# Kernel optimization log

Hardware: AMD Instinct MI355X
Metric: run time of the kernel (lower is better)

## Reference

```python
import jax, jax.numpy as jnp
import numpy as np

EPS = 1e-5

def _bn(x, g, b, m, v):
    # inference batchnorm: (x - mean) * rsqrt(var + eps) * gamma + beta
    return (x - m) * jax.lax.rsqrt(v + EPS) * g + b

def _relu6(x):
    return jnp.clip(x, 0.0, 6.0)

def setup_inputs() -> dict:
    key = jax.random.key(0)
    ks = jax.random.split(key, 20)
    N, Cin, Cout, K = 200000, 32, 32, 9  # K = 3^2 kernel offsets (dimension=2)
    H = int(round(Cin * 6))              # hidden = in_channels * expand_ratio = 192
    inp = {}
    inp["feats"] = jax.random.normal(ks[0], (N, Cin), jnp.float32)
    # rulebook neighbor map: -1 means no active neighbor at that kernel offset
    inp["neighbor_idx"] = jax.random.randint(ks[1], (N, K), -1, N, dtype=jnp.int32)
    # ME convs have bias=False by default
    inp["W1"] = jax.random.normal(ks[2], (Cin, H), jnp.float32) * 0.05
    inp["W2"] = jax.random.normal(ks[3], (K, H), jnp.float32) * 0.05   # channelwise (depthwise) kernel
    inp["W3"] = jax.random.normal(ks[4], (H, Cout), jnp.float32) * 0.05
    for i, (name, c) in enumerate([("1", H), ("2", H), ("3", Cout)]):
        base = 5 + 4 * i
        inp["g" + name] = 1.0 + 0.1 * jax.random.normal(ks[base], (c,), jnp.float32)
        inp["b" + name] = 0.1 * jax.random.normal(ks[base + 1], (c,), jnp.float32)
        inp["m" + name] = 0.1 * jax.random.normal(ks[base + 2], (c,), jnp.float32)
        inp["v" + name] = jax.random.uniform(ks[base + 3], (c,), jnp.float32, 0.5, 1.5)
    return inp

def _depthwise_sparse_conv(x, neighbor_idx, W2):
    # x: [N, H], neighbor_idx: [N, K] (-1 = missing), W2: [K, H]
    K = W2.shape[0]
    acc = jnp.zeros_like(x)
    safe = jnp.maximum(neighbor_idx, 0)
    valid = (neighbor_idx >= 0)
    for k in range(K):  # small fixed kernel loop; each gather streams [N, H]
        g = jnp.where(valid[:, k:k + 1], x[safe[:, k]], 0.0)
        acc = acc + g * W2[k]
    return acc

def reference(feats, neighbor_idx, W1, W2, W3,
              g1, b1, m1, v1, g2, b2, m2, v2, g3, b3, m3, v3):
    identity = feats
    x = _relu6(_bn(feats @ W1, g1, b1, m1, v1))          # 1x1 expand conv
    x = _depthwise_sparse_conv(x, neighbor_idx, W2)       # 3x3 depthwise sparse conv
    x = _relu6(_bn(x, g2, b2, m2, v2))
    x = _bn(x @ W3, g3, b3, m3, v3)                       # 1x1 project conv
    return x + identity                                   # residual (in==out, stride==1)
```

## Files before the change

kernel.cpp:

```cpp
#include <hip/hip_runtime.h>

#define EPS 1e-5f

typedef __bf16 bf16x8 __attribute__((ext_vector_type(8)));
typedef float f32x4 __attribute__((ext_vector_type(4)));

union BF8 { bf16x8 v; unsigned short u[8]; uint4 q; };

__device__ inline unsigned short f32_to_bf16(float f) {
    unsigned u = __builtin_bit_cast(unsigned, f);
    return (unsigned short)((u + 0x7FFFu + ((u >> 16) & 1u)) >> 16);
}
__device__ inline float bf16_lo(unsigned u) { return __builtin_bit_cast(float, u << 16); }
__device__ inline float bf16_hi(unsigned u) { return __builtin_bit_cast(float, u & 0xFFFF0000u); }
__device__ inline float relu6f(float x) { return fminf(fmaxf(x, 0.f), 6.f); }

__global__ __launch_bounds__(256) void k1_expand(
    const float* __restrict__ feats, const float* __restrict__ W1,
    const float* __restrict__ g1, const float* __restrict__ b1,
    const float* __restrict__ m1, const float* __restrict__ v1,
    unsigned short* __restrict__ x1, int N)
{
    __shared__ __align__(16) unsigned short w1t[192 * 40];
    __shared__ __align__(16) unsigned short aT[64 * 40];
    __shared__ __align__(16) unsigned short outT[64 * 200];
    __shared__ float sL[192], bL[192];
    const int tid = threadIdx.x;
    const int rowbase = blockIdx.x * 64;

    if (tid < 192) {
        float s = g1[tid] * rsqrtf(v1[tid] + EPS);
        sL[tid] = s;
        bL[tid] = b1[tid] - m1[tid] * s;
    }

#pragma unroll
    for (int j = 0; j < 6; ++j) {
        int f = (j * 256 + tid) * 4;
        float4 w = *(const float4*)(W1 + f);
        int k = f / 192, n = f % 192;
        w1t[(n + 0) * 40 + k] = f32_to_bf16(w.x);
        w1t[(n + 1) * 40 + k] = f32_to_bf16(w.y);
        w1t[(n + 2) * 40 + k] = f32_to_bf16(w.z);
        w1t[(n + 3) * 40 + k] = f32_to_bf16(w.w);
    }

    {
        int r = tid >> 2, c = (tid & 3) * 8;
        int gr = rowbase + r;
        float4 f0 = {0.f,0.f,0.f,0.f}, f1 = {0.f,0.f,0.f,0.f};
        if (gr < N) {
            f0 = *(const float4*)(feats + (size_t)gr * 32 + c);
            f1 = *(const float4*)(feats + (size_t)gr * 32 + c + 4);
        }
        BF8 p;
        p.u[0] = f32_to_bf16(f0.x); p.u[1] = f32_to_bf16(f0.y);
        p.u[2] = f32_to_bf16(f0.z); p.u[3] = f32_to_bf16(f0.w);
        p.u[4] = f32_to_bf16(f1.x); p.u[5] = f32_to_bf16(f1.y);
        p.u[6] = f32_to_bf16(f1.z); p.u[7] = f32_to_bf16(f1.w);
        *(uint4*)(&aT[r * 40 + c]) = p.q;
    }
    __syncthreads();

    const int lane = tid & 63, wave = tid >> 6;
    const int m = lane & 15, q = lane >> 4;

    bf16x8 af = *(const bf16x8*)(&aT[(wave * 16 + m) * 40 + q * 8]);

    f32x4 acc[12];
#pragma unroll
    for (int t = 0; t < 12; ++t) {
        bf16x8 bf = *(const bf16x8*)(&w1t[(16 * t + m) * 40 + q * 8]);
        f32x4 z = {0.f, 0.f, 0.f, 0.f};
        acc[t] = __builtin_amdgcn_mfma_f32_16x16x32_bf16(af, bf, z, 0, 0, 0);
    }

#pragma unroll
    for (int t = 0; t < 12; ++t) {
        int c = 16 * t + m;
        float s = sL[c], bb = bL[c];
#pragma unroll
        for (int i = 0; i < 4; ++i) {
            int r = wave * 16 + q * 4 + i;
            outT[r * 200 + c] = f32_to_bf16(relu6f(fmaf(acc[t][i], s, bb)));
        }
    }
    __syncthreads();

#pragma unroll
    for (int j = 0; j < 6; ++j) {
        int i = j * 256 + tid;
        int r = i / 24, c = i % 24;
        int gr = rowbase + r;
        if (gr < N)
            *(uint4*)(x1 + (size_t)gr * 192 + c * 8) = *(const uint4*)(&outT[r * 200 + c * 8]);
    }
}

__global__ __launch_bounds__(192) void k2_fused(
    const unsigned short* __restrict__ x1, const int* __restrict__ nbr,
    const float* __restrict__ W2, const float* __restrict__ W3,
    const float* __restrict__ g2, const float* __restrict__ b2,
    const float* __restrict__ m2, const float* __restrict__ v2,
    const float* __restrict__ g3, const float* __restrict__ b3,
    const float* __restrict__ m3, const float* __restrict__ v3,
    const float* __restrict__ feats, float* __restrict__ out, int N)
{
    __shared__ __align__(16) unsigned short x2L[48 * 200];
    __shared__ __align__(16) int nbrL[48 * 12];
    const int tid = threadIdx.x;
    const int rowbase = blockIdx.x * 48;

    for (int i = tid; i < 432; i += 192) {
        int r = i / 9, k = i - r * 9;
        int n = rowbase + r;
        nbrL[r * 12 + k] = (n < N) ? nbr[(size_t)n * 9 + k] : -1;
    }

    const int cg = tid % 48;
    const int slot = tid / 48;
    const int c0 = cg * 4;

    float w2[9][4];
#pragma unroll
    for (int k = 0; k < 9; ++k) {
        float4 w = *(const float4*)(W2 + k * 192 + c0);
        w2[k][0] = w.x; w2[k][1] = w.y; w2[k][2] = w.z; w2[k][3] = w.w;
    }
    float s2[4], bb2[4];
#pragma unroll
    for (int j = 0; j < 4; ++j) {
        int c = c0 + j;
        s2[j] = g2[c] * rsqrtf(v2[c] + EPS);
        bb2[j] = b2[c] - m2[c] * s2[j];
    }
    __syncthreads();

#pragma unroll
    for (int it = 0; it < 12; ++it) {
        int r = it * 4 + slot;
        const int* nb = &nbrL[r * 12];
        int4 n03 = *(const int4*)nb;
        int4 n47 = *(const int4*)(nb + 4);
        int n8 = nb[8];
        int idx[9] = {n03.x, n03.y, n03.z, n03.w, n47.x, n47.y, n47.z, n47.w, n8};
        uint2 gv[9];
#pragma unroll
        for (int k = 0; k < 9; ++k) {
            int safe = idx[k] < 0 ? 0 : idx[k];
            gv[k] = *(const uint2*)(x1 + (size_t)safe * 192 + c0);
        }
        float a0 = 0.f, a1 = 0.f, a2 = 0.f, a3 = 0.f;
#pragma unroll
        for (int k = 0; k < 9; ++k) {
            unsigned ux = idx[k] >= 0 ? gv[k].x : 0u;
            unsigned uy = idx[k] >= 0 ? gv[k].y : 0u;
            a0 = fmaf(bf16_lo(ux), w2[k][0], a0);
            a1 = fmaf(bf16_hi(ux), w2[k][1], a1);
            a2 = fmaf(bf16_lo(uy), w2[k][2], a2);
            a3 = fmaf(bf16_hi(uy), w2[k][3], a3);
        }
        a0 = relu6f(fmaf(a0, s2[0], bb2[0]));
        a1 = relu6f(fmaf(a1, s2[1], bb2[1]));
        a2 = relu6f(fmaf(a2, s2[2], bb2[2]));
        a3 = relu6f(fmaf(a3, s2[3], bb2[3]));
        uint2 pk;
        pk.x = (unsigned)f32_to_bf16(a0) | ((unsigned)f32_to_bf16(a1) << 16);
        pk.y = (unsigned)f32_to_bf16(a2) | ((unsigned)f32_to_bf16(a3) << 16);
        *(uint2*)(&x2L[r * 200 + c0]) = pk;
    }
    __syncthreads();

    const int lane = tid & 63;
    const int wave = tid >> 6;
    const int m = lane & 15;
    const int q = lane >> 4;

    bf16x8 bfrag[12];
#pragma unroll
    for (int s = 0; s < 6; ++s)
#pragma unroll
        for (int t = 0; t < 2; ++t) {
            BF8 tmp;
#pragma unroll
            for (int j = 0; j < 8; ++j)
                tmp.u[j] = f32_to_bf16(W3[(32 * s + q * 8 + j) * 32 + 16 * t + m]);
            bfrag[s * 2 + t] = tmp.v;
        }

    f32x4 acc0 = {0.f, 0.f, 0.f, 0.f}, acc1 = {0.f, 0.f, 0.f, 0.f};
    const int rw = wave * 16;
#pragma unroll
    for (int s = 0; s < 6; ++s) {
        bf16x8 a = *reinterpret_cast<const bf16x8*>(&x2L[(rw + m) * 200 + 32 * s + q * 8]);
        acc0 = __builtin_amdgcn_mfma_f32_16x16x32_bf16(a, bfrag[s * 2 + 0], acc0, 0, 0, 0);
        acc1 = __builtin_amdgcn_mfma_f32_16x16x32_bf16(a, bfrag[s * 2 + 1], acc1, 0, 0, 0);
    }

#pragma unroll
    for (int t = 0; t < 2; ++t) {
        f32x4 acc = (t == 0) ? acc0 : acc1;
        int c = 16 * t + m;
        float s3  = g3[c] * rsqrtf(v3[c] + EPS);
        float bb3 = b3[c] - m3[c] * s3;
#pragma unroll
        for (int i = 0; i < 4; ++i) {
            int r = rowbase + rw + q * 4 + i;
            if (r < N) {
                int o = r * 32 + c;
                out[o] = fmaf(acc[i], s3, bb3) + feats[o];
            }
        }
    }
}

extern "C" void kernel_launch(void* const* d_in, const int* in_sizes, int n_in,
                              void* d_out, int out_size, void* d_ws, size_t ws_size,
                              hipStream_t stream) {
    const float* feats = (const float*)d_in[0];
    const int*   nbr   = (const int*)d_in[1];
    const float* W1    = (const float*)d_in[2];
    const float* W2    = (const float*)d_in[3];
    const float* W3    = (const float*)d_in[4];
    const float* g1 = (const float*)d_in[5];
    const float* b1 = (const float*)d_in[6];
    const float* m1 = (const float*)d_in[7];
    const float* v1 = (const float*)d_in[8];
    const float* g2 = (const float*)d_in[9];
    const float* b2 = (const float*)d_in[10];
    const float* m2 = (const float*)d_in[11];
    const float* v2 = (const float*)d_in[12];
    const float* g3 = (const float*)d_in[13];
    const float* b3 = (const float*)d_in[14];
    const float* m3 = (const float*)d_in[15];
    const float* v3 = (const float*)d_in[16];
    float* out = (float*)d_out;

    const int N = in_sizes[0] / 32;
    unsigned short* x1 = (unsigned short*)d_ws;

    k1_expand<<<dim3((N + 63) / 64), dim3(256), 0, stream>>>(
        feats, W1, g1, b1, m1, v1, x1, N);
    k2_fused<<<dim3((N + 47) / 48), dim3(192), 0, stream>>>(
        x1, nbr, W2, W3, g2, b2, m2, v2, g3, b3, m3, v3, feats, out, N);
}
```

Baseline: 237.1 us.

## Precompute bf16 weights and folded BN constants in a prep kernel; pair gather rows

Adds a small prep kernel that converts W1 and W3 to transposed bf16 and folds all three batchnorms into scale/bias arrays in workspace. This removes the per-block weight conversion and BN rsqrt work from the expand and fused kernels. The gather loop in k2 now handles two rows per iteration with precomputed byte offsets, giving more independent loads in flight. The cost is an extra kernel launch, global rather than LDS reads for weights, and higher register pressure in k2.

```diff
diff --git a/kernel.cpp b/kernel.cpp
--- a/kernel.cpp
+++ b/kernel.cpp
@@ -15,35 +15,50 @@
 __device__ inline float bf16_hi(unsigned u) { return __builtin_bit_cast(float, u & 0xFFFF0000u); }
 __device__ inline float relu6f(float x) { return fminf(fmaxf(x, 0.f), 6.f); }
 
-__global__ __launch_bounds__(256) void k1_expand(
-    const float* __restrict__ feats, const float* __restrict__ W1,
+__global__ __launch_bounds__(256) void k0_prep(
+    const float* __restrict__ W1, const float* __restrict__ W3,
     const float* __restrict__ g1, const float* __restrict__ b1,
     const float* __restrict__ m1, const float* __restrict__ v1,
-    unsigned short* __restrict__ x1, int N)
+    const float* __restrict__ g2, const float* __restrict__ b2,
+    const float* __restrict__ m2, const float* __restrict__ v2,
+    const float* __restrict__ g3, const float* __restrict__ b3,
+    const float* __restrict__ m3, const float* __restrict__ v3,
+    unsigned short* __restrict__ w1t, unsigned short* __restrict__ w3t,
+    float* __restrict__ bnc)
 {
-    __shared__ __align__(16) unsigned short w1t[192 * 40];
+    const int gtid = blockIdx.x * 256 + threadIdx.x;
+    const int gstr = gridDim.x * 256;
+    for (int i = gtid; i < 6144; i += gstr) {
+        int n = i >> 5, k = i & 31;
+        w1t[i] = f32_to_bf16(W1[k * 192 + n]);
+    }
+    for (int i = gtid; i < 6144; i += gstr) {
+        int n = i / 192, k = i - n * 192;
+        w3t[i] = f32_to_bf16(W3[k * 32 + n]);
+    }
+    if (blockIdx.x == 0) {
+        int t = threadIdx.x;
+        if (t < 192) {
+            float s = g1[t] * rsqrtf(v1[t] + EPS);
+            bnc[t] = s; bnc[192 + t] = b1[t] - m1[t] * s;
+            float u = g2[t] * rsqrtf(v2[t] + EPS);
+            bnc[384 + t] = u; bnc[576 + t] = b2[t] - m2[t] * u;
+            if (t < 32) {
+                float w = g3[t] * rsqrtf(v3[t] + EPS);
+                bnc[768 + t] = w; bnc[800 + t] = b3[t] - m3[t] * w;
+            }
+        }
+    }
+}
+
+__global__ __launch_bounds__(256) void k1_expand(
+    const float* __restrict__ feats, const unsigned short* __restrict__ w1t,
+    const float* __restrict__ bnc, unsigned short* __restrict__ x1, int N)
+{
     __shared__ __align__(16) unsigned short aT[64 * 40];
     __shared__ __align__(16) unsigned short outT[64 * 200];
-    __shared__ float sL[192], bL[192];
     const int tid = threadIdx.x;
     const int rowbase = blockIdx.x * 64;
-
-    if (tid < 192) {
-        float s = g1[tid] * rsqrtf(v1[tid] + EPS);
-        sL[tid] = s;
-        bL[tid] = b1[tid] - m1[tid] * s;
-    }
-
-#pragma unroll
-    for (int j = 0; j < 6; ++j) {
-        int f = (j * 256 + tid) * 4;
-        float4 w = *(const float4*)(W1 + f);
-        int k = f / 192, n = f % 192;
-        w1t[(n + 0) * 40 + k] = f32_to_bf16(w.x);
-        w1t[(n + 1) * 40 + k] = f32_to_bf16(w.y);
-        w1t[(n + 2) * 40 + k] = f32_to_bf16(w.z);
-        w1t[(n + 3) * 40 + k] = f32_to_bf16(w.w);
-    }
 
     {
         int r = tid >> 2, c = (tid & 3) * 8;
@@ -70,7 +85,7 @@
     f32x4 acc[12];
 #pragma unroll
     for (int t = 0; t < 12; ++t) {
-        bf16x8 bf = *(const bf16x8*)(&w1t[(16 * t + m) * 40 + q * 8]);
+        bf16x8 bf = *(const bf16x8*)(w1t + (16 * t + m) * 32 + q * 8);
         f32x4 z = {0.f, 0.f, 0.f, 0.f};
         acc[t] = __builtin_amdgcn_mfma_f32_16x16x32_bf16(af, bf, z, 0, 0, 0);
     }
@@ -78,7 +93,7 @@
 #pragma unroll
     for (int t = 0; t < 12; ++t) {
         int c = 16 * t + m;
-        float s = sL[c], bb = bL[c];
+        float s = bnc[c], bb = bnc[192 + c];
 #pragma unroll
         for (int i = 0; i < 4; ++i) {
             int r = wave * 16 + q * 4 + i;
@@ -99,75 +114,84 @@
 
 __global__ __launch_bounds__(192) void k2_fused(
     const unsigned short* __restrict__ x1, const int* __restrict__ nbr,
-    const float* __restrict__ W2, const float* __restrict__ W3,
-    const float* __restrict__ g2, const float* __restrict__ b2,
-    const float* __restrict__ m2, const float* __restrict__ v2,
-    const float* __restrict__ g3, const float* __restrict__ b3,
-    const float* __restrict__ m3, const float* __restrict__ v3,
-    const float* __restrict__ feats, float* __restrict__ out, int N)
+    const float* __restrict__ W2, const unsigned short* __restrict__ w3t,
+    const float* __restrict__ bnc, const float* __restrict__ feats,
+    float* __restrict__ out, int N)
 {
     __shared__ __align__(16) unsigned short x2L[48 * 200];
-    __shared__ __align__(16) int nbrL[48 * 12];
+    __shared__ __align__(16) int offL[48 * 12];
     const int tid = threadIdx.x;
     const int rowbase = blockIdx.x * 48;
 
     for (int i = tid; i < 432; i += 192) {
         int r = i / 9, k = i - r * 9;
         int n = rowbase + r;
-        nbrL[r * 12 + k] = (n < N) ? nbr[(size_t)n * 9 + k] : -1;
+        int idx = (n < N) ? nbr[(size_t)n * 9 + k] : -1;
+        offL[r * 12 + k] = (idx < 0) ? -1 : idx * 384;
     }
 
     const int cg = tid % 48;
     const int slot = tid / 48;
     const int c0 = cg * 4;
-
-    float w2[9][4];
+    const char* x1b = (const char*)x1 + c0 * 2;
+
+    float w2v[9][4];
 #pragma unroll
     for (int k = 0; k < 9; ++k) {
         float4 w = *(const float4*)(W2 + k * 192 + c0);
-        w2[k][0] = w.x; w2[k][1] = w.y; w2[k][2] = w.z; w2[k][3] = w.w;
-    }
-    float s2[4], bb2[4];
-#pragma unroll
-    for (int j = 0; j < 4; ++j) {
-        int c = c0 + j;
-        s2[j] = g2[c] * rsqrtf(v2[c] + EPS);
-        bb2[j] = b2[c] - m2[c] * s2[j];
-    }
-    __syncthreads();
-
-#pragma unroll
-    for (int it = 0; it < 12; ++it) {
-        int r = it * 4 + slot;
-        const int* nb = &nbrL[r * 12];
-        int4 n03 = *(const int4*)nb;
-        int4 n47 = *(const int4*)(nb + 4);
-        int n8 = nb[8];
-        int idx[9] = {n03.x, n03.y, n03.z, n03.w, n47.x, n47.y, n47.z, n47.w, n8};
-        uint2 gv[9];
+        w2v[k][0] = w.x; w2v[k][1] = w.y; w2v[k][2] = w.z; w2v[k][3] = w.w;
+    }
+    float4 s2 = *(const float4*)(bnc + 384 + c0);
+    float4 bb2 = *(const float4*)(bnc + 576 + c0);
+    __syncthreads();
+
+#pragma unroll
+    for (int it = 0; it < 6; ++it) {
+        int r0 = it * 8 + slot, r1 = r0 + 4;
+        const int* nA = &offL[r0 * 12];
+        const int* nB = &offL[r1 * 12];
+        int4 a03 = *(const int4*)nA; int4 a47 = *(const int4*)(nA + 4); int a8 = nA[8];
+        int4 b03 = *(const int4*)nB; int4 b47 = *(const int4*)(nB + 4); int b8 = nB[8];
+        int offA[9] = {a03.x, a03.y, a03.z, a03.w, a47.x, a47.y, a47.z, a47.w, a8};
+        int offB[9] = {b03.x, b03.y, b03.z, b03.w, b47.x, b47.y, b47.z, b47.w, b8};
+        uint2 gA[9], gB[9];
 #pragma unroll
         for (int k = 0; k < 9; ++k) {
-            int safe = idx[k] < 0 ? 0 : idx[k];
-            gv[k] = *(const uint2*)(x1 + (size_t)safe * 192 + c0);
+            gA[k] = *(const uint2*)(x1b + (offA[k] < 0 ? 0 : offA[k]));
+            gB[k] = *(const uint2*)(x1b + (offB[k] < 0 ? 0 : offB[k]));
         }
         float a0 = 0.f, a1 = 0.f, a2 = 0.f, a3 = 0.f;
+        float c0f = 0.f, c1 = 0.f, c2 = 0.f, c3 = 0.f;
 #pragma unroll
         for (int k = 0; k < 9; ++k) {
-            unsigned ux = idx[k] >= 0 ? gv[k].x : 0u;
-            unsigned uy = idx[k] >= 0 ? gv[k].y : 0u;
-            a0 = fmaf(bf16_lo(ux), w2[k][0], a0);
-            a1 = fmaf(bf16_hi(ux), w2[k][1], a1);
-            a2 = fmaf(bf16_lo(uy), w2[k][2], a2);
-            a3 = fmaf(bf16_hi(uy), w2[k][3], a3);
-        }
-        a0 = relu6f(fmaf(a0, s2[0], bb2[0]));
-        a1 = relu6f(fmaf(a1, s2[1], bb2[1]));
-        a2 = relu6f(fmaf(a2, s2[2], bb2[2]));
-        a3 = relu6f(fmaf(a3, s2[3], bb2[3]));
-        uint2 pk;
-        pk.x = (unsigned)f32_to_bf16(a0) | ((unsigned)f32_to_bf16(a1) << 16);
-        pk.y = (unsigned)f32_to_bf16(a2) | ((unsigned)f32_to_bf16(a3) << 16);
-        *(uint2*)(&x2L[r * 200 + c0]) = pk;
+            unsigned ax = offA[k] >= 0 ? gA[k].x : 0u;
+            unsigned ay = offA[k] >= 0 ? gA[k].y : 0u;
+            a0 = fmaf(bf16_lo(ax), w2v[k][0], a0);
+            a1 = fmaf(bf16_hi(ax), w2v[k][1], a1);
+            a2 = fmaf(bf16_lo(ay), w2v[k][2], a2);
+            a3 = fmaf(bf16_hi(ay), w2v[k][3], a3);
+            unsigned bx = offB[k] >= 0 ? gB[k].x : 0u;
+            unsigned by = offB[k] >= 0 ? gB[k].y : 0u;
+            c0f = fmaf(bf16_lo(bx), w2v[k][0], c0f);
+            c1  = fmaf(bf16_hi(bx), w2v[k][1], c1);
+            c2  = fmaf(bf16_lo(by), w2v[k][2], c2);
+            c3  = fmaf(bf16_hi(by), w2v[k][3], c3);
+        }
+        a0 = relu6f(fmaf(a0, s2.x, bb2.x));
+        a1 = relu6f(fmaf(a1, s2.y, bb2.y));
+        a2 = relu6f(fmaf(a2, s2.z, bb2.z));
+        a3 = relu6f(fmaf(a3, s2.w, bb2.w));
+        c0f = relu6f(fmaf(c0f, s2.x, bb2.x));
+        c1  = relu6f(fmaf(c1,  s2.y, bb2.y));
+        c2  = relu6f(fmaf(c2,  s2.z, bb2.z));
+        c3  = relu6f(fmaf(c3,  s2.w, bb2.w));
+        uint2 pA, pB;
+        pA.x = (unsigned)f32_to_bf16(a0) | ((unsigned)f32_to_bf16(a1) << 16);
+        pA.y = (unsigned)f32_to_bf16(a2) | ((unsigned)f32_to_bf16(a3) << 16);
+        pB.x = (unsigned)f32_to_bf16(c0f) | ((unsigned)f32_to_bf16(c1) << 16);
+        pB.y = (unsigned)f32_to_bf16(c2)  | ((unsigned)f32_to_bf16(c3) << 16);
+        *(uint2*)(&x2L[r0 * 200 + c0]) = pA;
+        *(uint2*)(&x2L[r1 * 200 + c0]) = pB;
     }
     __syncthreads();
 
@@ -180,13 +204,8 @@
 #pragma unroll
     for (int s = 0; s < 6; ++s)
 #pragma unroll
-        for (int t = 0; t < 2; ++t) {
-            BF8 tmp;
-#pragma unroll
-            for (int j = 0; j < 8; ++j)
-                tmp.u[j] = f32_to_bf16(W3[(32 * s + q * 8 + j) * 32 + 16 * t + m]);
-            bfrag[s * 2 + t] = tmp.v;
-        }
+        for (int t = 0; t < 2; ++t)
+            bfrag[s * 2 + t] = *(const bf16x8*)(w3t + (16 * t + m) * 192 + 32 * s + q * 8);
 
     f32x4 acc0 = {0.f, 0.f, 0.f, 0.f}, acc1 = {0.f, 0.f, 0.f, 0.f};
     const int rw = wave * 16;
@@ -201,8 +220,7 @@
     for (int t = 0; t < 2; ++t) {
         f32x4 acc = (t == 0) ? acc0 : acc1;
         int c = 16 * t + m;
-        float s3  = g3[c] * rsqrtf(v3[c] + EPS);
-        float bb3 = b3[c] - m3[c] * s3;
+        float s3 = bnc[768 + c], bb3 = bnc[800 + c];
 #pragma unroll
         for (int i = 0; i < 4; ++i) {
             int r = rowbase + rw + q * 4 + i;
@@ -237,10 +255,17 @@
     float* out = (float*)d_out;
 
     const int N = in_sizes[0] / 32;
-    unsigned short* x1 = (unsigned short*)d_ws;
-
+
+    char* ws = (char*)d_ws;
+    unsigned short* x1  = (unsigned short*)ws;
+    unsigned short* w1t = (unsigned short*)(ws + (size_t)N * 192 * 2);
+    unsigned short* w3t = w1t + 6144;
+    float*          bnc = (float*)(w3t + 6144);
+
+    k0_prep<<<dim3(32), dim3(256), 0, stream>>>(
+        W1, W3, g1, b1, m1, v1, g2, b2, m2, v2, g3, b3, m3, v3, w1t, w3t, bnc);
     k1_expand<<<dim3((N + 63) / 64), dim3(256), 0, stream>>>(
-        feats, W1, g1, b1, m1, v1, x1, N);
+        feats, w1t, bnc, x1, N);
     k2_fused<<<dim3((N + 47) / 48), dim3(192), 0, stream>>>(
-        x1, nbr, W2, W3, g2, b2, m2, v2, g3, b3, m3, v3, feats, out, N);
-}
+        x1, nbr, W2, w3t, bnc, feats, out, N);
+}
```

Result: faster. 229.6 us (-3.2%).
